# Kernel tuning notes

Hardware: AMD Instinct MI355X
Metric: run time of the kernel (lower is better)

The kernel has to match this reference:

```python
import jax, jax.numpy as jnp
import numpy as np

EMBED = 2048
NUM_EXPERTS = 64
TOP_K = 8


def setup_inputs() -> dict:
    key = jax.random.key(0)
    k1, k2, k3 = jax.random.split(key, 3)
    inputs = jax.random.normal(k1, (8, 4096, EMBED), dtype=jnp.float32)
    # nn.Linear(embed_size, num_experts): weight [num_experts, embed_size], bias [num_experts]
    W = jax.random.normal(k2, (NUM_EXPERTS, EMBED), dtype=jnp.float32) / np.sqrt(EMBED)
    b = jax.random.normal(k3, (NUM_EXPERTS,), dtype=jnp.float32) * 0.01
    return {"inputs": inputs, "W": W, "b": b}


def reference(inputs, W, b):
    # Linear projection: [B, S, E] x [E, N] -> [B, S, N]
    logits = jnp.einsum('bse,ne->bsn', inputs, W) + b
    # top-k selection along expert axis
    _, indices = jax.lax.top_k(logits, TOP_K)  # [B, S, K] int32
    # scatter mask: 1 at selected experts (one_hot sum == scatter_ of ones)
    mask = jax.nn.one_hot(indices, NUM_EXPERTS, dtype=jnp.bool_).any(axis=-2)  # [B, S, N]
    # masked_fill(-inf) + softmax -> probs only on selected experts
    masked = jnp.where(mask, logits, -jnp.inf)
    probs = jax.nn.softmax(masked, axis=-1)
    return probs, indices
```

## Files before the change

### kernel.cpp

```cpp
#include <hip/hip_runtime.h>
#include <cmath>

#define NTOK 32768
#define EMB  2048
#define NEXP 64
#define TOPK 8
#define BT   64
#define KC   64
#define NCH  (EMB / KC)
#define TAU  1e-4f

typedef __attribute__((ext_vector_type(8))) short bf16x8;
typedef __attribute__((ext_vector_type(4))) float f32x4;

union U4 { unsigned int u[4]; bf16x8 v; };

__device__ unsigned short g_wl[NCH][12288];
__device__ float g_wt4[EMB * 64];

static __device__ __forceinline__ float uf(unsigned int x) { return __uint_as_float(x); }
static __device__ __forceinline__ unsigned int fu(float x) { return __float_as_uint(x); }

__device__ __forceinline__ void gld16(const void* g, void* lds) {
    __builtin_amdgcn_global_load_lds(
        (const __attribute__((address_space(1))) void*)g,
        (__attribute__((address_space(3))) void*)lds,
        16, 0, 0);
}

__global__ __launch_bounds__(512) void wsplit(const float* __restrict__ W) {
    const int ch  = blockIdx.x;
    const int tid = threadIdx.x;
    const int er = tid >> 3, kk = (tid >> 2) & 1, q = tid & 3;
    const int k0 = ch * KC + kk * 32 + q * 8;
    const float* src = &W[(size_t)er * EMB + k0];
    float x[8];
    #pragma unroll
    for (int j = 0; j < 8; ++j) x[j] = src[j];
    #pragma unroll
    for (int j = 0; j < 8; ++j) {
        const int k = k0 + j;
        g_wt4[(k >> 2) * 256 + er * 4 + (k & 3)] = x[j];
    }
    unsigned int P[3][4];
    #pragma unroll
    for (int m = 0; m < 4; ++m) {
        float x0 = x[2*m], x1 = x[2*m+1];
        unsigned int u0 = fu(x0), u1 = fu(x1);
        P[0][m] = (u0 >> 16) | (u1 & 0xffff0000u);
        float r0 = x0 - uf(u0 & 0xffff0000u), r1 = x1 - uf(u1 & 0xffff0000u);
        unsigned int w0 = fu(r0), w1 = fu(r1);
        P[1][m] = (w0 >> 16) | (w1 & 0xffff0000u);
        float s0 = r0 - uf(w0 & 0xffff0000u), s1 = r1 - uf(w1 & 0xffff0000u);
        P[2][m] = (fu(s0) >> 16) | (fu(s1) & 0xffff0000u);
    }
    #pragma unroll
    for (int p = 0; p < 3; ++p) {
        unsigned short* d = &g_wl[ch][((p*2 + kk)*4 + q)*512 + er*8];
        *(uint4*)(void*)d = make_uint4(P[p][0], P[p][1], P[p][2], P[p][3]);
    }
}

__global__ __launch_bounds__(512, 2) void router_mx(
    const float* __restrict__ X,
    const float* __restrict__ W,
    const float* __restrict__ Bv,
    float* __restrict__ out)
{
    __shared__ __align__(16) unsigned char smem[81920];
    float* xsBase          = (float*)smem;
    unsigned short* wsBase = (unsigned short*)(smem + 32768);
    float* lg              = (float*)smem;

    const int tid  = threadIdx.x;
    const int lane = tid & 63;
    const int w    = tid >> 6;
    const int tg   = w >> 1;
    const int eh   = w & 1;
    const int eL   = lane & 15;
    const int q    = lane >> 4;
    const int t0   = blockIdx.x * BT;

    f32x4 am[2], ac[2];
    #pragma unroll
    for (int t = 0; t < 2; ++t) {
        am[t] = (f32x4){0.f, 0.f, 0.f, 0.f};
        ac[t] = (f32x4){0.f, 0.f, 0.f, 0.f};
    }

    auto stage = [&](int ch, int buf) {
        float* xd = xsBase + buf * 4096;
        #pragma unroll
        for (int j = 0; j < 2; ++j) {
            const int rb  = (w * 2 + j) * 4;
            const int row = rb + (lane >> 4);
            const int gl  = (lane & 15) ^ (row & 7);
            gld16(&X[(size_t)(t0 + row) * EMB + ch * KC + 4 * gl], xd + rb * 64);
        }
        unsigned short* wd = wsBase + buf * 12288;
        const unsigned short* wsrc = &g_wl[ch][0];
        #pragma unroll
        for (int j = 0; j < 3; ++j) {
            const int o = (w * 3 + j) * 512;
            gld16(wsrc + o + lane * 8, wd + o);
        }
    };

    auto compute = [&](int buf) {
        const float* xb          = xsBase + buf * 4096;
        const unsigned short* wb = wsBase + buf * 12288;
        const int row = tg * 16 + eL;
        #pragma unroll
        for (int kk = 0; kk < 2; ++kk) {
            bf16x8 Bf0[3], Bf1[3];
            #pragma unroll
            for (int p = 0; p < 3; ++p) {
                const int seg = ((p * 2 + kk) * 4 + q) * 512;
                Bf0[p] = *(const bf16x8*)(const void*)(wb + seg + (eh * 32 + eL) * 8);
                Bf1[p] = *(const bf16x8*)(const void*)(wb + seg + (eh * 32 + 16 + eL) * 8);
            }
            const int g0 = kk * 8 + ((2 * q) ^ (row & 7));
            const int g1 = kk * 8 + ((2 * q + 1) ^ (row & 7));
            const float4 aL = *(const float4*)&xb[row * 64 + 4 * g0];
            const float4 aH = *(const float4*)&xb[row * 64 + 4 * g1];
            U4 A1, A2, A3;
            const float e0[8] = {aL.x, aL.y, aL.z, aL.w, aH.x, aH.y, aH.z, aH.w};
            #pragma unroll
            for (int m = 0; m < 4; ++m) {
                float x0 = e0[2*m], x1 = e0[2*m+1];
                unsigned int u0 = fu(x0), u1 = fu(x1);
                A1.u[m] = (u0 >> 16) | (u1 & 0xffff0000u);
                float r0 = x0 - uf(u0 & 0xffff0000u), r1 = x1 - uf(u1 & 0xffff0000u);
                unsigned int w0 = fu(r0), w1 = fu(r1);
                A2.u[m] = (w0 >> 16) | (w1 & 0xffff0000u);
                float s0 = r0 - uf(w0 & 0xffff0000u), s1 = r1 - uf(w1 & 0xffff0000u);
                A3.u[m] = (fu(s0) >> 16) | (fu(s1) & 0xffff0000u);
            }
            am[0] = __builtin_amdgcn_mfma_f32_16x16x32_bf16(A1.v, Bf0[0], am[0], 0,0,0);
            ac[0] = __builtin_amdgcn_mfma_f32_16x16x32_bf16(A1.v, Bf0[1], ac[0], 0,0,0);
            ac[0] = __builtin_amdgcn_mfma_f32_16x16x32_bf16(A2.v, Bf0[0], ac[0], 0,0,0);
            ac[0] = __builtin_amdgcn_mfma_f32_16x16x32_bf16(A1.v, Bf0[2], ac[0], 0,0,0);
            ac[0] = __builtin_amdgcn_mfma_f32_16x16x32_bf16(A2.v, Bf0[1], ac[0], 0,0,0);
            ac[0] = __builtin_amdgcn_mfma_f32_16x16x32_bf16(A3.v, Bf0[0], ac[0], 0,0,0);
            am[1] = __builtin_amdgcn_mfma_f32_16x16x32_bf16(A1.v, Bf1[0], am[1], 0,0,0);
            ac[1] = __builtin_amdgcn_mfma_f32_16x16x32_bf16(A1.v, Bf1[1], ac[1], 0,0,0);
            ac[1] = __builtin_amdgcn_mfma_f32_16x16x32_bf16(A2.v, Bf1[0], ac[1], 0,0,0);
            ac[1] = __builtin_amdgcn_mfma_f32_16x16x32_bf16(A1.v, Bf1[2], ac[1], 0,0,0);
            ac[1] = __builtin_amdgcn_mfma_f32_16x16x32_bf16(A2.v, Bf1[1], ac[1], 0,0,0);
            ac[1] = __builtin_amdgcn_mfma_f32_16x16x32_bf16(A3.v, Bf1[0], ac[1], 0,0,0);
        }
    };

    stage(0, 0);
    for (int ch = 0; ch < NCH; ++ch) {
        const int cur = ch & 1;
        if (ch + 1 < NCH) {
            stage(ch + 1, cur ^ 1);
            asm volatile("s_waitcnt vmcnt(5)" ::: "memory");
        } else {
            asm volatile("s_waitcnt vmcnt(0)" ::: "memory");
        }
        __builtin_amdgcn_s_barrier();
        asm volatile("" ::: "memory");
        compute(cur);
        asm volatile("" ::: "memory");
        __builtin_amdgcn_s_barrier();
    }

    float* probs = out;
    float* idxo  = out + (size_t)NTOK * NEXP;
    const float bb0 = Bv[eh * 32 + eL];
    const float bb1 = Bv[eh * 32 + 16 + eL];
    #pragma unroll
    for (int cc = 0; cc < 2; ++cc) {
        const int e = eh * 32 + cc * 16 + eL;
        const float bbv = cc ? bb1 : bb0;
        #pragma unroll
        for (int i = 0; i < 4; ++i) {
            const int r = tg * 16 + q * 4 + i;
            lg[r * 66 + e] = (am[cc][i] + ac[cc][i]) + bbv;
        }
    }
    __syncthreads();

    auto slowToken = [&](int Tg) {
        const float* xr = X + (size_t)Tg * EMB;
        double s0 = 0.0, s1 = 0.0, s2 = 0.0, s3 = 0.0;
        for (int k = 0; k < EMB; k += 8) {
            const float4 xa = *(const float4*)&xr[k];
            const float4 xb = *(const float4*)&xr[k + 4];
            const float4 wa = *(const float4*)&g_wt4[(k >> 2) * 256 + lane * 4];
            const float4 wb = *(const float4*)&g_wt4[((k >> 2) + 1) * 256 + lane * 4];
            s0 += (double)xa.x * wa.x + (double)xb.x * wb.x;
            s1 += (double)xa.y * wa.y + (double)xb.y * wb.y;
            s2 += (double)xa.z * wa.z + (double)xb.z * wb.z;
            s3 += (double)xa.w * wa.w + (double)xb.w * wb.w;
        }
        double ex = (double)Bv[lane] + ((s0 + s1) + (s2 + s3));
        bool selb = false; int myrank = 0;
        double m0d = 0.0; float ss = 0.f;
        #pragma unroll
        for (int it = 0; it < TOPK; ++it) {
            double bv = selb ? -1.0e300 : ex; int be = lane;
            #pragma unroll
            for (int off = 1; off <= 32; off <<= 1) {
                const double ov = __shfl_xor(bv, off, 64);
                const int    oe = __shfl_xor(be, off, 64);
                if (ov > bv || (ov == bv && oe < be)) { bv = ov; be = oe; }
            }
            if (it == 0) m0d = bv;
            ss += __expf((float)(bv - m0d));
            if (lane == be) { selb = true; myrank = it; }
        }
        probs[(size_t)Tg * NEXP + lane] = selb ? __expf((float)(ex - m0d)) / ss : 0.f;
        if (selb) idxo[(size_t)Tg * TOPK + myrank] = (float)lane;
    };

    #pragma unroll
    for (int i = 0; i < 2; ++i) {
        const int T = w * 8 + i * 4 + q;
        float v[4];
        #pragma unroll
        for (int c = 0; c < 4; ++c) v[c] = lg[T * 66 + c * 16 + eL];

        unsigned sel = 0;
        float m0 = 0.f, ssum = 0.f, prev = 0.f, mingap = 1e30f;
        int myIdx = 0;
        #pragma unroll
        for (int it = 0; it <= TOPK; ++it) {
            float bv = -1e30f; int be = 1 << 30;
            #pragma unroll
            for (int c = 0; c < 4; ++c)
                if (!((sel >> c) & 1) && v[c] > bv) { bv = v[c]; be = c * 16 + eL; }
            float gv = bv; int ge = be;
            #pragma unroll
            for (int off = 1; off <= 8; off <<= 1) {
                const float ov = __shfl_xor(gv, off, 64);
                const int   oe = __shfl_xor(ge, off, 64);
                if (ov > gv || (ov == gv && oe < ge)) { gv = ov; ge = oe; }
            }
            if (it == 0) m0 = gv;
            else mingap = fminf(mingap, prev - gv);
            prev = gv;
            if (it < TOPK) {
                ssum += __expf(gv - m0);
                if ((ge & 15) == eL) sel |= 1u << (ge >> 4);
                if (eL == it) myIdx = ge;
            }
        }
        const int Tg = t0 + T;
        const float inv = 1.0f / ssum;
        #pragma unroll
        for (int c = 0; c < 4; ++c) {
            const float p = ((sel >> c) & 1) ? __expf(v[c] - m0) * inv : 0.0f;
            probs[(size_t)Tg * NEXP + c * 16 + eL] = p;
        }
        if (eL < TOPK) idxo[(size_t)Tg * TOPK + eL] = (float)myIdx;

        const unsigned long long fb = __ballot(mingap < TAU);
        for (int q2 = 0; q2 < 4; ++q2)
            if ((fb >> (q2 * 16)) & 1) slowToken(t0 + w * 8 + i * 4 + q2);
    }
}

extern "C" void kernel_launch(void* const* d_in, const int* in_sizes, int n_in,
                              void* d_out, int out_size, void* d_ws, size_t ws_size,
                              hipStream_t stream) {
    const float* X = (const float*)d_in[0];
    const float* W = (const float*)d_in[1];
    const float* B = (const float*)d_in[2];
    wsplit<<<NCH, 512, 0, stream>>>(W);
    router_mx<<<NTOK / BT, 512, 0, stream>>>(X, W, B, (float*)d_out);
}
```

Measured before the change: 498.0 us.

## Drop LDS staging: each wave loads X directly and reads split weights from global

The router kernel no longer double-buffers X and the split bf16 weights through shared memory with block barriers. Each wave now owns 16 tokens and all 64 experts. It loads its X rows straight into registers with register double-buffering and reads the three-way bf16 weight split directly from global memory, which is mostly cache-resident. The epilogue takes the logits straight from the MFMA accumulators instead of going through an LDS transpose. This removes the barriers and the LDS traffic, but each wave now issues more global weight loads and holds more accumulator registers.

```diff
diff --git a/kernel.cpp b/kernel.cpp
--- a/kernel.cpp
+++ b/kernel.cpp
@@ -5,7 +5,6 @@
 #define EMB  2048
 #define NEXP 64
 #define TOPK 8
-#define BT   64
 #define KC   64
 #define NCH  (EMB / KC)
 #define TAU  1e-4f
@@ -20,13 +19,6 @@
 
 static __device__ __forceinline__ float uf(unsigned int x) { return __uint_as_float(x); }
 static __device__ __forceinline__ unsigned int fu(float x) { return __float_as_uint(x); }
-
-__device__ __forceinline__ void gld16(const void* g, void* lds) {
-    __builtin_amdgcn_global_load_lds(
-        (const __attribute__((address_space(1))) void*)g,
-        (__attribute__((address_space(3))) void*)lds,
-        16, 0, 0);
-}
 
 __global__ __launch_bounds__(512) void wsplit(const float* __restrict__ W) {
     const int ch  = blockIdx.x;
@@ -61,68 +53,42 @@
     }
 }
 
-__global__ __launch_bounds__(512, 2) void router_mx(
+__global__ __launch_bounds__(256, 2) void router_ws(
     const float* __restrict__ X,
     const float* __restrict__ W,
     const float* __restrict__ Bv,
     float* __restrict__ out)
 {
-    __shared__ __align__(16) unsigned char smem[81920];
-    float* xsBase          = (float*)smem;
-    unsigned short* wsBase = (unsigned short*)(smem + 32768);
-    float* lg              = (float*)smem;
-
-    const int tid  = threadIdx.x;
-    const int lane = tid & 63;
-    const int w    = tid >> 6;
-    const int tg   = w >> 1;
-    const int eh   = w & 1;
+    const int lane = threadIdx.x & 63;
+    const int wv   = threadIdx.x >> 6;
     const int eL   = lane & 15;
     const int q    = lane >> 4;
-    const int t0   = blockIdx.x * BT;
-
-    f32x4 am[2], ac[2];
-    #pragma unroll
-    for (int t = 0; t < 2; ++t) {
+    const int tok0 = (blockIdx.x * 4 + wv) * 16;
+
+    f32x4 am[4], ac[4];
+    #pragma unroll
+    for (int t = 0; t < 4; ++t) {
         am[t] = (f32x4){0.f, 0.f, 0.f, 0.f};
         ac[t] = (f32x4){0.f, 0.f, 0.f, 0.f};
     }
 
-    auto stage = [&](int ch, int buf) {
-        float* xd = xsBase + buf * 4096;
-        #pragma unroll
-        for (int j = 0; j < 2; ++j) {
-            const int rb  = (w * 2 + j) * 4;
-            const int row = rb + (lane >> 4);
-            const int gl  = (lane & 15) ^ (row & 7);
-            gld16(&X[(size_t)(t0 + row) * EMB + ch * KC + 4 * gl], xd + rb * 64);
-        }
-        unsigned short* wd = wsBase + buf * 12288;
-        const unsigned short* wsrc = &g_wl[ch][0];
-        #pragma unroll
-        for (int j = 0; j < 3; ++j) {
-            const int o = (w * 3 + j) * 512;
-            gld16(wsrc + o + lane * 8, wd + o);
+    const float* xrow = X + (size_t)(tok0 + eL) * EMB + q * 8;
+
+    float4 xA[2][2], xB[2][2];
+    auto ldX = [&](int ch, float4 (&xv)[2][2]) {
+        #pragma unroll
+        for (int kk = 0; kk < 2; ++kk) {
+            #pragma unroll
+            for (int h = 0; h < 2; ++h)
+                xv[kk][h] = *(const float4*)&xrow[ch * 64 + kk * 32 + h * 4];
         }
     };
 
-    auto compute = [&](int buf) {
-        const float* xb          = xsBase + buf * 4096;
-        const unsigned short* wb = wsBase + buf * 12288;
-        const int row = tg * 16 + eL;
+    auto doChunk = [&](int ch, const float4 (&xv)[2][2]) {
+        const unsigned short* wb = &g_wl[ch][0];
         #pragma unroll
         for (int kk = 0; kk < 2; ++kk) {
-            bf16x8 Bf0[3], Bf1[3];
-            #pragma unroll
-            for (int p = 0; p < 3; ++p) {
-                const int seg = ((p * 2 + kk) * 4 + q) * 512;
-                Bf0[p] = *(const bf16x8*)(const void*)(wb + seg + (eh * 32 + eL) * 8);
-                Bf1[p] = *(const bf16x8*)(const void*)(wb + seg + (eh * 32 + 16 + eL) * 8);
-            }
-            const int g0 = kk * 8 + ((2 * q) ^ (row & 7));
-            const int g1 = kk * 8 + ((2 * q + 1) ^ (row & 7));
-            const float4 aL = *(const float4*)&xb[row * 64 + 4 * g0];
-            const float4 aH = *(const float4*)&xb[row * 64 + 4 * g1];
+            const float4 aL = xv[kk][0], aH = xv[kk][1];
             U4 A1, A2, A3;
             const float e0[8] = {aL.x, aL.y, aL.z, aL.w, aH.x, aH.y, aH.z, aH.w};
             #pragma unroll
@@ -136,52 +102,35 @@
                 float s0 = r0 - uf(w0 & 0xffff0000u), s1 = r1 - uf(w1 & 0xffff0000u);
                 A3.u[m] = (fu(s0) >> 16) | (fu(s1) & 0xffff0000u);
             }
-            am[0] = __builtin_amdgcn_mfma_f32_16x16x32_bf16(A1.v, Bf0[0], am[0], 0,0,0);
-            ac[0] = __builtin_amdgcn_mfma_f32_16x16x32_bf16(A1.v, Bf0[1], ac[0], 0,0,0);
-            ac[0] = __builtin_amdgcn_mfma_f32_16x16x32_bf16(A2.v, Bf0[0], ac[0], 0,0,0);
-            ac[0] = __builtin_amdgcn_mfma_f32_16x16x32_bf16(A1.v, Bf0[2], ac[0], 0,0,0);
-            ac[0] = __builtin_amdgcn_mfma_f32_16x16x32_bf16(A2.v, Bf0[1], ac[0], 0,0,0);
-            ac[0] = __builtin_amdgcn_mfma_f32_16x16x32_bf16(A3.v, Bf0[0], ac[0], 0,0,0);
-            am[1] = __builtin_amdgcn_mfma_f32_16x16x32_bf16(A1.v, Bf1[0], am[1], 0,0,0);
-            ac[1] = __builtin_amdgcn_mfma_f32_16x16x32_bf16(A1.v, Bf1[1], ac[1], 0,0,0);
-            ac[1] = __builtin_amdgcn_mfma_f32_16x16x32_bf16(A2.v, Bf1[0], ac[1], 0,0,0);
-            ac[1] = __builtin_amdgcn_mfma_f32_16x16x32_bf16(A1.v, Bf1[2], ac[1], 0,0,0);
-            ac[1] = __builtin_amdgcn_mfma_f32_16x16x32_bf16(A2.v, Bf1[1], ac[1], 0,0,0);
-            ac[1] = __builtin_amdgcn_mfma_f32_16x16x32_bf16(A3.v, Bf1[0], ac[1], 0,0,0);
+            #pragma unroll
+            for (int cc = 0; cc < 4; ++cc) {
+                const int fo = q * 512 + (cc * 16 + eL) * 8;
+                const bf16x8 b0 = *(const bf16x8*)(const void*)(wb + (0*2 + kk) * 2048 + fo);
+                const bf16x8 b1 = *(const bf16x8*)(const void*)(wb + (1*2 + kk) * 2048 + fo);
+                const bf16x8 b2 = *(const bf16x8*)(const void*)(wb + (2*2 + kk) * 2048 + fo);
+                am[cc] = __builtin_amdgcn_mfma_f32_16x16x32_bf16(A1.v, b0, am[cc], 0,0,0);
+                ac[cc] = __builtin_amdgcn_mfma_f32_16x16x32_bf16(A1.v, b1, ac[cc], 0,0,0);
+                ac[cc] = __builtin_amdgcn_mfma_f32_16x16x32_bf16(A2.v, b0, ac[cc], 0,0,0);
+                ac[cc] = __builtin_amdgcn_mfma_f32_16x16x32_bf16(A1.v, b2, ac[cc], 0,0,0);
+                ac[cc] = __builtin_amdgcn_mfma_f32_16x16x32_bf16(A2.v, b1, ac[cc], 0,0,0);
+                ac[cc] = __builtin_amdgcn_mfma_f32_16x16x32_bf16(A3.v, b0, ac[cc], 0,0,0);
+            }
         }
     };
 
-    stage(0, 0);
-    for (int ch = 0; ch < NCH; ++ch) {
-        const int cur = ch & 1;
-        if (ch + 1 < NCH) {
-            stage(ch + 1, cur ^ 1);
-            asm volatile("s_waitcnt vmcnt(5)" ::: "memory");
-        } else {
-            asm volatile("s_waitcnt vmcnt(0)" ::: "memory");
-        }
-        __builtin_amdgcn_s_barrier();
-        asm volatile("" ::: "memory");
-        compute(cur);
-        asm volatile("" ::: "memory");
-        __builtin_amdgcn_s_barrier();
+    ldX(0, xA);
+    for (int ch = 0; ch < NCH; ch += 2) {
+        ldX(ch + 1, xB);
+        doChunk(ch, xA);
+        if (ch + 2 < NCH) ldX(ch + 2, xA);
+        doChunk(ch + 1, xB);
     }
 
     float* probs = out;
     float* idxo  = out + (size_t)NTOK * NEXP;
-    const float bb0 = Bv[eh * 32 + eL];
-    const float bb1 = Bv[eh * 32 + 16 + eL];
-    #pragma unroll
-    for (int cc = 0; cc < 2; ++cc) {
-        const int e = eh * 32 + cc * 16 + eL;
-        const float bbv = cc ? bb1 : bb0;
-        #pragma unroll
-        for (int i = 0; i < 4; ++i) {
-            const int r = tg * 16 + q * 4 + i;
-            lg[r * 66 + e] = (am[cc][i] + ac[cc][i]) + bbv;
-        }
-    }
-    __syncthreads();
+    float bb[4];
+    #pragma unroll
+    for (int c = 0; c < 4; ++c) bb[c] = Bv[c * 16 + eL];
 
     auto slowToken = [&](int Tg) {
         const float* xr = X + (size_t)Tg * EMB;
@@ -217,11 +166,10 @@
     };
 
     #pragma unroll
-    for (int i = 0; i < 2; ++i) {
-        const int T = w * 8 + i * 4 + q;
+    for (int i = 0; i < 4; ++i) {
         float v[4];
         #pragma unroll
-        for (int c = 0; c < 4; ++c) v[c] = lg[T * 66 + c * 16 + eL];
+        for (int c = 0; c < 4; ++c) v[c] = (am[c][i] + ac[c][i]) + bb[c];
 
         unsigned sel = 0;
         float m0 = 0.f, ssum = 0.f, prev = 0.f, mingap = 1e30f;
@@ -248,7 +196,7 @@
                 if (eL == it) myIdx = ge;
             }
         }
-        const int Tg = t0 + T;
+        const int Tg = tok0 + q * 4 + i;
         const float inv = 1.0f / ssum;
         #pragma unroll
         for (int c = 0; c < 4; ++c) {
@@ -259,7 +207,7 @@
 
         const unsigned long long fb = __ballot(mingap < TAU);
         for (int q2 = 0; q2 < 4; ++q2)
-            if ((fb >> (q2 * 16)) & 1) slowToken(t0 + w * 8 + i * 4 + q2);
+            if ((fb >> (q2 * 16)) & 1) slowToken(tok0 + q2 * 4 + i);
     }
 }
 
@@ -270,5 +218,5 @@
     const float* W = (const float*)d_in[1];
     const float* B = (const float*)d_in[2];
     wsplit<<<NCH, 512, 0, stream>>>(W);
-    router_mx<<<NTOK / BT, 512, 0, stream>>>(X, W, B, (float*)d_out);
+    router_ws<<<NTOK / 64, 256, 0, stream>>>(X, W, B, (float*)d_out);
 }
```

Result: slower. 590.8 us (+18.6%).
